# Optimization experiments

Hardware: AMD Instinct MI355X
Metric: run time of the kernel (lower is better)

The kernel has to match this reference:

```python
import jax, jax.numpy as jnp
import numpy as np

B, S, D, H = 4, 2048, 1024, 16
HD = D // H  # 64


def setup_inputs() -> dict:
    key = jax.random.key(0)
    k1, k2, k3, k4, k5 = jax.random.split(key, 5)
    scale = 0.02
    return {
        "hidden_states": jax.random.normal(k1, (B, S, D), dtype=jnp.float32),
        "c_attn_w": jax.random.normal(k2, (D, 3 * D), dtype=jnp.float32) * scale,
        "c_attn_b": jax.random.normal(k3, (3 * D,), dtype=jnp.float32) * scale,
        "c_proj_w": jax.random.normal(k4, (D, D), dtype=jnp.float32) * scale,
        "c_proj_b": jax.random.normal(k5, (D,), dtype=jnp.float32) * scale,
    }


def reference(hidden_states, c_attn_w, c_attn_b, c_proj_w, c_proj_b):
    b, s, d = hidden_states.shape
    # Conv1D: x @ W + b, fused QKV
    qkv = hidden_states @ c_attn_w + c_attn_b  # [b, s, 3d]
    q, k, v = jnp.split(qkv, 3, axis=-1)
    # split heads -> [b, h, s, hd]
    def split_heads(x):
        return x.reshape(b, s, H, HD).transpose(0, 2, 1, 3)
    q, k, v = split_heads(q), split_heads(k), split_heads(v)
    # scaled dot-product attention with causal mask (eager GPT-2 math)
    scores = jnp.einsum("bhqd,bhkd->bhqk", q, k) / jnp.asarray(HD ** 0.5, q.dtype)
    causal = jnp.tril(jnp.ones((s, s), dtype=bool))  # [s, s]
    mask_value = jnp.asarray(jnp.finfo(scores.dtype).min, scores.dtype)
    scores = jnp.where(causal[None, None, :, :], scores, mask_value)
    attn = jax.nn.softmax(scores, axis=-1)
    out = jnp.einsum("bhqk,bhkd->bhqd", attn, v)  # [b, h, s, hd]
    out = out.transpose(0, 2, 1, 3).reshape(b, s, d)  # merge heads
    out = out @ c_proj_w + c_proj_b
    return out
```

## Files before the change

kernel.cpp:

```cpp
#include <hip/hip_runtime.h>
#include <hip/hip_bf16.h>
#include <stdint.h>

#define B_ 4
#define S_ 2048
#define D_ 1024
#define H_ 16
#define HD_ 64

typedef __bf16 bf16_t;
typedef bf16_t bf16x8 __attribute__((ext_vector_type(8)));
typedef bf16_t bf16x4 __attribute__((ext_vector_type(4)));
typedef float f32x4 __attribute__((ext_vector_type(4)));
typedef float f32x16 __attribute__((ext_vector_type(16)));

__device__ __forceinline__ bf16x8 cvt8(f32x4 lo, f32x4 hi) {
  bf16x8 r;
#pragma unroll
  for (int i = 0; i < 4; i++) {
    r[i] = (bf16_t)lo[i];
    r[i + 4] = (bf16_t)hi[i];
  }
  return r;
}

__device__ __forceinline__ void async_lds16(const bf16_t* g, bf16_t* l) {
  __builtin_amdgcn_global_load_lds(
      (const __attribute__((address_space(1))) void*)g,
      (__attribute__((address_space(3))) void*)l, 16, 0, 0);
}

__device__ __forceinline__ uint32_t pk2(float a, float b) {
  union {
    bf16_t h[2];
    uint32_t u;
  } x;
  x.h[0] = (bf16_t)a;
  x.h[1] = (bf16_t)b;
  return x.u;
}

__device__ __forceinline__ void swap32(uint32_t& a, uint32_t& b) {
  asm("v_permlane32_swap_b32 %0, %1" : "+v"(a), "+v"(b));
}

union PAU {
  uint32_t w[4];
  bf16x8 v;
};

__global__ __launch_bounds__(256) void cvt_f32_bf16(
    const float* __restrict__ in, bf16_t* __restrict__ out) {
  size_t i = ((size_t)blockIdx.x * 256 + threadIdx.x) * 8;
  f32x4 lo = *(const f32x4*)(in + i);
  f32x4 hi = *(const f32x4*)(in + i + 4);
  *(bf16x8*)(out + i) = cvt8(lo, hi);
}

__global__ void transpose_cvt(const float* __restrict__ in,
                              bf16_t* __restrict__ out, int R, int C) {
  __shared__ bf16_t tile[32][33];
  int c0 = blockIdx.x * 32, r0 = blockIdx.y * 32;
  int tx = threadIdx.x, ty = threadIdx.y;
  for (int i = ty; i < 32; i += 8)
    tile[i][tx] = (bf16_t)in[(size_t)(r0 + i) * C + c0 + tx];
  __syncthreads();
  for (int i = ty; i < 32; i += 8)
    out[(size_t)(c0 + i) * R + r0 + tx] = tile[tx][i];
}

__global__ __launch_bounds__(256) void gemm_bt(
    const void* __restrict__ A, const bf16_t* __restrict__ BT,
    const float* __restrict__ bias, float* __restrict__ Cout,
    bf16_t* __restrict__ qws, bf16_t* __restrict__ kws,
    bf16_t* __restrict__ vws, int M, int Nw, int K, int mode, int a_is_f32,
    size_t a_off) {
  __shared__ bf16_t As[128 * 32];
  __shared__ bf16_t Bs[128 * 32];
  const int tid = threadIdx.x;
  const int wave = tid >> 6, lane = tid & 63;
  const int quad = lane >> 4, tn = lane & 15;
  const int m_blk = blockIdx.y * 128, n_blk = blockIdx.x * 128;
  const int wm = (wave >> 1) * 64, wn = (wave & 1) * 64;

  f32x4 acc[4][4] = {};

  const int srow = wave * 32 + (lane >> 2);
  const int scol = (lane & 3) * 8;
  size_t aoff = a_off + (size_t)(m_blk + srow) * K + scol;
  const bf16_t* gb = BT + (size_t)(n_blk + srow) * K + scol;
  bf16_t* lbB0 = &Bs[wave * 1024];
  bf16_t* lbB1 = &Bs[wave * 1024 + 512];
  bf16_t* laA0 = &As[wave * 1024];
  bf16_t* laA1 = &As[wave * 1024 + 512];

  for (int k0 = 0; k0 < K; k0 += 32) {
    async_lds16(gb, lbB0);
    async_lds16(gb + (size_t)16 * K, lbB1);
    if (a_is_f32) {
      const float* gaf = (const float*)A + aoff;
      f32x4 a00 = *(const f32x4*)gaf;
      f32x4 a01 = *(const f32x4*)(gaf + 4);
      f32x4 a10 = *(const f32x4*)(gaf + (size_t)16 * K);
      f32x4 a11 = *(const f32x4*)(gaf + (size_t)16 * K + 4);
      *(bf16x8*)&As[srow * 32 + scol] = cvt8(a00, a01);
      *(bf16x8*)&As[(srow + 16) * 32 + scol] = cvt8(a10, a11);
    } else {
      const bf16_t* ga = (const bf16_t*)A + aoff;
      async_lds16(ga, laA0);
      async_lds16(ga + (size_t)16 * K, laA1);
    }
    aoff += 32;
    gb += 32;
    __syncthreads();

    bf16x8 af[4], bfr[4];
#pragma unroll
    for (int i = 0; i < 4; i++)
      af[i] = *(const bf16x8*)&As[(wm + i * 16 + tn) * 32 + quad * 8];
#pragma unroll
    for (int i = 0; i < 4; i++)
      bfr[i] = *(const bf16x8*)&Bs[(wn + i * 16 + tn) * 32 + quad * 8];
#pragma unroll
    for (int mi = 0; mi < 4; mi++)
#pragma unroll
      for (int ni = 0; ni < 4; ni++)
        acc[mi][ni] = __builtin_amdgcn_mfma_f32_16x16x32_bf16(af[mi], bfr[ni],
                                                              acc[mi][ni], 0, 0, 0);
    __syncthreads();
  }

  if (mode == 0) {
#pragma unroll
    for (int ni = 0; ni < 4; ni++) {
      int n = n_blk + wn + ni * 16 + tn;
      float bv = bias[n];
#pragma unroll
      for (int mi = 0; mi < 4; mi++)
#pragma unroll
        for (int r = 0; r < 4; r++) {
          int m = m_blk + wm + mi * 16 + quad * 4 + r;
          Cout[(size_t)m * Nw + n] = acc[mi][ni][r] + bv;
        }
    }
  } else {
#pragma unroll
    for (int ni = 0; ni < 4; ni++) {
      int n = n_blk + wn + ni * 16 + tn;
      int sec = n >> 10;
      int hn = n & 1023;
      int hh = hn >> 6, hd = hn & 63;
      float bv = bias[n];
      if (sec == 2) {
#pragma unroll
        for (int mi = 0; mi < 4; mi++) {
          int m = m_blk + wm + mi * 16 + quad * 4;
          int bb = m >> 11, s = m & 2047;
          bf16x4 pk;
#pragma unroll
          for (int r = 0; r < 4; r++) pk[r] = (bf16_t)(acc[mi][ni][r] + bv);
          *(bf16x4*)&vws[((size_t)(bb * H_ + hh) * HD_ + hd) * S_ + s] = pk;
        }
      } else {
        bf16_t* dst = (sec == 0) ? qws : kws;
#pragma unroll
        for (int mi = 0; mi < 4; mi++)
#pragma unroll
          for (int r = 0; r < 4; r++) {
            int m = m_blk + wm + mi * 16 + quad * 4 + r;
            int bb = m >> 11, s = m & 2047;
            dst[((size_t)(bb * H_ + hh) * S_ + s) * HD_ + hd] =
                (bf16_t)(acc[mi][ni][r] + bv);
          }
      }
    }
  }
}

__global__ __launch_bounds__(512, 2) void attn_kernel(
    const bf16_t* __restrict__ Qw, const bf16_t* __restrict__ Kw,
    const bf16_t* __restrict__ VTw, bf16_t* __restrict__ Ow) {
  __shared__ bf16_t Ks[2][64 * 64];
  __shared__ bf16_t Vt[2][64 * 64];

  const int tid = threadIdx.x;
  const int wave = tid >> 6, lane = tid & 63;
  const int lq = lane & 31;
  const int h = lane >> 5;
  const int qoff = h * 4;
  const int bid = blockIdx.x;
  const int j = bid >> 3;
  const int bh = (bid & 7) * 8 + (j >> 2);
  const int pj = j & 3;

  const bf16_t* Qb = Qw + (size_t)bh * S_ * HD_;
  const bf16_t* Kb = Kw + (size_t)bh * S_ * HD_;
  const bf16_t* VTb = VTw + (size_t)bh * HD_ * S_;

  const float kScale = 0.125f * 1.44269504088896f;

  bf16x8 onesf;
#pragma unroll
  for (int jj = 0; jj < 8; jj++) onesf[jj] = (bf16_t)1.0f;

  const float NEG = -30000.0f;
  const int b = bh >> 4, hh = bh & 15;

  const int srow = wave * 8 + (lane >> 3);
  const int sslot = lane & 7;
  const bf16_t* kp = Kb + (size_t)srow * HD_ + (sslot ^ (srow & 7)) * 8;
  const bf16_t* vp = VTb + (size_t)srow * S_ + (sslot ^ (srow & 7)) * 8;

#define STAGE(buf, kt)                                                 \
  do {                                                                 \
    async_lds16(kp + (size_t)(kt) * (64 * HD_), &Ks[buf][wave * 512]); \
    async_lds16(vp + (size_t)(kt) * 64, &Vt[buf][wave * 512]);         \
  } while (0)

  for (int task = 0; task < 2; task++) {
    const int qt = task == 0 ? (7 - pj) : pj;
    const int qb = qt * 256;
    const int qa = qb + ((lq >> 3) << 6) + wave * 8 + (lq & 7);

    bf16x8 qf[4];
#pragma unroll
    for (int kg = 0; kg < 4; kg++) {
      bf16x8 v = *(const bf16x8*)&Qb[(size_t)qa * HD_ + kg * 16 + h * 8];
#pragma unroll
      for (int jj = 0; jj < 8; jj++) v[jj] = (bf16_t)((float)v[jj] * kScale);
      qf[kg] = v;
    }

    f32x16 o0 = {}, o1 = {};
    f32x16 ls = {};
    float mrow = NEG;

    const int kt_max = (qb + 255) >> 6;

    if (task) __syncthreads();
    STAGE(0, 0);

    for (int kt = 0; kt <= kt_max; kt++) {
      __syncthreads();
      if (kt < kt_max) STAGE((kt + 1) & 1, kt + 1);

      const bf16_t* KsB = Ks[kt & 1];
      const bf16_t* VtB = Vt[kt & 1];
      const int rsl = lq & 7;

      f32x16 st0 = {}, st1 = {};
      __builtin_amdgcn_s_setprio(1);
#pragma unroll
      for (int kg = 0; kg < 4; kg++) {
        const int slot = kg * 2 + h;
        bf16x8 kf0 = *(const bf16x8*)&KsB[lq * 64 + ((slot ^ rsl) * 8)];
        bf16x8 kf1 = *(const bf16x8*)&KsB[(32 + lq) * 64 + ((slot ^ rsl) * 8)];
        st0 = __builtin_amdgcn_mfma_f32_32x32x16_bf16(kf0, qf[kg], st0, 0, 0, 0);
        st1 = __builtin_amdgcn_mfma_f32_32x32x16_bf16(kf1, qf[kg], st1, 0, 0, 0);
      }
      __builtin_amdgcn_s_setprio(0);
      if (kt * 64 + 63 > qb) {
#pragma unroll
        for (int r = 0; r < 16; r++) {
          int key0 = kt * 64 + (r & 3) + 8 * (r >> 2) + qoff;
          if (key0 > qa) st0[r] = NEG;
          if (key0 + 32 > qa) st1[r] = NEG;
        }
      }
      float m8[8];
#pragma unroll
      for (int i = 0; i < 4; i++) {
        m8[i] = fmaxf(fmaxf(st0[4 * i], st0[4 * i + 1]),
                      fmaxf(st0[4 * i + 2], st0[4 * i + 3]));
        m8[4 + i] = fmaxf(fmaxf(st1[4 * i], st1[4 * i + 1]),
                          fmaxf(st1[4 * i + 2], st1[4 * i + 3]));
      }
      float mx = fmaxf(fmaxf(fmaxf(m8[0], m8[1]), fmaxf(m8[2], m8[3])),
                       fmaxf(fmaxf(m8[4], m8[5]), fmaxf(m8[6], m8[7])));
      mx = fmaxf(mx, __shfl_xor(mx, 32, 64));

      if (__any(mx > mrow + 8.f)) {
        float mnew = fmaxf(mrow, mx);
        float alpha = exp2f(mrow - mnew);
        mrow = mnew;
#pragma unroll
        for (int r = 0; r < 16; r++) {
          float ar = __shfl(alpha, (r & 3) + 8 * (r >> 2) + qoff, 64);
          o0[r] *= ar;
          o1[r] *= ar;
          ls[r] *= ar;
        }
      }
#pragma unroll
      for (int r = 0; r < 16; r++) {
        st0[r] = exp2f(st0[r] - mrow);
        st1[r] = exp2f(st1[r] - mrow);
      }

      PAU pa[4];
      {
        uint32_t w[8];
#pragma unroll
        for (int i = 0; i < 8; i++) w[i] = pk2(st0[2 * i], st0[2 * i + 1]);
        swap32(w[0], w[2]);
        swap32(w[1], w[3]);
        swap32(w[4], w[6]);
        swap32(w[5], w[7]);
        pa[0].w[0] = w[0]; pa[0].w[1] = w[1]; pa[0].w[2] = w[2]; pa[0].w[3] = w[3];
        pa[1].w[0] = w[4]; pa[1].w[1] = w[5]; pa[1].w[2] = w[6]; pa[1].w[3] = w[7];
#pragma unroll
        for (int i = 0; i < 8; i++) w[i] = pk2(st1[2 * i], st1[2 * i + 1]);
        swap32(w[0], w[2]);
        swap32(w[1], w[3]);
        swap32(w[4], w[6]);
        swap32(w[5], w[7]);
        pa[2].w[0] = w[0]; pa[2].w[1] = w[1]; pa[2].w[2] = w[2]; pa[2].w[3] = w[3];
        pa[3].w[0] = w[4]; pa[3].w[1] = w[5]; pa[3].w[2] = w[6]; pa[3].w[3] = w[7];
      }

      __builtin_amdgcn_s_setprio(1);
#pragma unroll
      for (int kg = 0; kg < 4; kg++) {
        const int slot = kg * 2 + h;
        bf16x8 vf0 = *(const bf16x8*)&VtB[lq * 64 + ((slot ^ rsl) * 8)];
        bf16x8 vf1 = *(const bf16x8*)&VtB[(32 + lq) * 64 + ((slot ^ rsl) * 8)];
        o0 = __builtin_amdgcn_mfma_f32_32x32x16_bf16(pa[kg].v, vf0, o0, 0, 0, 0);
        o1 = __builtin_amdgcn_mfma_f32_32x32x16_bf16(pa[kg].v, vf1, o1, 0, 0, 0);
        ls = __builtin_amdgcn_mfma_f32_32x32x16_bf16(pa[kg].v, onesf, ls, 0, 0, 0);
      }
      __builtin_amdgcn_s_setprio(0);
    }

#pragma unroll
    for (int r = 0; r < 16; r++) {
      int qr = (r & 3) + 8 * (r >> 2) + qoff;
      int q = qb + ((qr >> 3) << 6) + wave * 8 + (qr & 7);
      float inv = 1.f / fmaxf(ls[r], 1e-30f);
      bf16_t* dst = Ow + (size_t)(b * S_ + q) * D_ + hh * HD_;
      dst[lq] = (bf16_t)(o0[r] * inv);
      dst[32 + lq] = (bf16_t)(o1[r] * inv);
    }
  }
#undef STAGE
}

extern "C" void kernel_launch(void* const* d_in, const int* in_sizes, int n_in,
                              void* d_out, int out_size, void* d_ws,
                              size_t ws_size, hipStream_t stream) {
  const float* hidden = nullptr;
  const float* attn_w = nullptr;
  const float* attn_b = nullptr;
  const float* proj_w = nullptr;
  const float* proj_b = nullptr;
  for (int i = 0; i < n_in; ++i) {
    switch (in_sizes[i]) {
      case 8388608: hidden = (const float*)d_in[i]; break;
      case 3145728: attn_w = (const float*)d_in[i]; break;
      case 3072:    attn_b = (const float*)d_in[i]; break;
      case 1048576: proj_w = (const float*)d_in[i]; break;
      case 1024:    proj_b = (const float*)d_in[i]; break;
      default: break;
    }
  }
  if (!hidden) hidden = (const float*)d_in[0];
  if (!attn_w) attn_w = (const float*)d_in[1];
  if (!attn_b) attn_b = (const float*)d_in[2];
  if (!proj_w) proj_w = (const float*)d_in[3];
  if (!proj_b) proj_b = (const float*)d_in[4];
  float* out = (float*)d_out;

  char* ws = (char*)d_ws;
  const size_t AWS_B = (size_t)B_ * S_ * D_ * 2;
  const size_t QKV_E = (size_t)B_ * H_ * S_ * HD_;

  bf16_t* aws = (bf16_t*)ws;
  bf16_t* wT1 = (bf16_t*)ws;
  bf16_t* qws = (bf16_t*)(ws + AWS_B);
  bf16_t* kws = qws + QKV_E;
  bf16_t* vws = kws + QKV_E;
  bf16_t* wT2 = qws;
  bf16_t* hb = (bf16_t*)d_out;

  cvt_f32_bf16<<<dim3(4096), 256, 0, stream>>>(hidden, hb);
  transpose_cvt<<<dim3(96, 32), dim3(32, 8), 0, stream>>>(attn_w, wT1, 1024, 3072);
  gemm_bt<<<dim3(24, 64), 256, 0, stream>>>(
      hb, wT1, attn_b, nullptr, qws, kws, vws, 8192, 3072, 1024, 1, 0, 0);
  attn_kernel<<<dim3(256), 512, 0, stream>>>(qws, kws, vws, aws);
  transpose_cvt<<<dim3(32, 32), dim3(32, 8), 0, stream>>>(proj_w, wT2, 1024, 1024);
  gemm_bt<<<dim3(8, 64), 256, 0, stream>>>(
      aws, wT2, proj_b, out, nullptr, nullptr, nullptr, 8192, 1024, 1024, 0, 0, 0);
}
```

Baseline: 286.8 us.

## Rewrite GEMM as 256x128 tile with triple-buffered async LDS pipeline and swizzle

Replaces the 128x128, K=32 single-buffered GEMM with a 512-thread 256x128 tile kernel using K=64 steps and a three-stage async global-to-LDS pipeline. It adds an XOR swizzle on LDS columns to avoid bank conflicts, and uses fine-grained vmcnt waits plus raised wave priority around the MFMA blocks. The aim is to hide global load latency, halve barriers per unit of work and raise operand reuse. In exchange it uses much more LDS (about 144KB), which limits occupancy, and the proj GEMM launches only 256 blocks.

```diff
diff --git a/kernel.cpp b/kernel.cpp
--- a/kernel.cpp
+++ b/kernel.cpp
@@ -69,92 +69,125 @@
     out[(size_t)(c0 + i) * R + r0 + tx] = tile[tx][i];
 }
 
-__global__ __launch_bounds__(256) void gemm_bt(
-    const void* __restrict__ A, const bf16_t* __restrict__ BT,
+__global__ __launch_bounds__(512, 2) void gemm256(
+    const bf16_t* __restrict__ Ab, const bf16_t* __restrict__ Bb,
     const float* __restrict__ bias, float* __restrict__ Cout,
     bf16_t* __restrict__ qws, bf16_t* __restrict__ kws,
-    bf16_t* __restrict__ vws, int M, int Nw, int K, int mode, int a_is_f32,
-    size_t a_off) {
-  __shared__ bf16_t As[128 * 32];
-  __shared__ bf16_t Bs[128 * 32];
+    bf16_t* __restrict__ vws, int M, int Nw, int K, int mode) {
+  __shared__ bf16_t As[3 * 256 * 64];
+  __shared__ bf16_t Bs[3 * 128 * 64];
   const int tid = threadIdx.x;
   const int wave = tid >> 6, lane = tid & 63;
   const int quad = lane >> 4, tn = lane & 15;
-  const int m_blk = blockIdx.y * 128, n_blk = blockIdx.x * 128;
-  const int wm = (wave >> 1) * 64, wn = (wave & 1) * 64;
-
-  f32x4 acc[4][4] = {};
-
-  const int srow = wave * 32 + (lane >> 2);
-  const int scol = (lane & 3) * 8;
-  size_t aoff = a_off + (size_t)(m_blk + srow) * K + scol;
-  const bf16_t* gb = BT + (size_t)(n_blk + srow) * K + scol;
-  bf16_t* lbB0 = &Bs[wave * 1024];
-  bf16_t* lbB1 = &Bs[wave * 1024 + 512];
-  bf16_t* laA0 = &As[wave * 1024];
-  bf16_t* laA1 = &As[wave * 1024 + 512];
-
-  for (int k0 = 0; k0 < K; k0 += 32) {
-    async_lds16(gb, lbB0);
-    async_lds16(gb + (size_t)16 * K, lbB1);
-    if (a_is_f32) {
-      const float* gaf = (const float*)A + aoff;
-      f32x4 a00 = *(const f32x4*)gaf;
-      f32x4 a01 = *(const f32x4*)(gaf + 4);
-      f32x4 a10 = *(const f32x4*)(gaf + (size_t)16 * K);
-      f32x4 a11 = *(const f32x4*)(gaf + (size_t)16 * K + 4);
-      *(bf16x8*)&As[srow * 32 + scol] = cvt8(a00, a01);
-      *(bf16x8*)&As[(srow + 16) * 32 + scol] = cvt8(a10, a11);
-    } else {
-      const bf16_t* ga = (const bf16_t*)A + aoff;
-      async_lds16(ga, laA0);
-      async_lds16(ga + (size_t)16 * K, laA1);
-    }
-    aoff += 32;
-    gb += 32;
-    __syncthreads();
-
-    bf16x8 af[4], bfr[4];
-#pragma unroll
-    for (int i = 0; i < 4; i++)
-      af[i] = *(const bf16x8*)&As[(wm + i * 16 + tn) * 32 + quad * 8];
-#pragma unroll
-    for (int i = 0; i < 4; i++)
-      bfr[i] = *(const bf16x8*)&Bs[(wn + i * 16 + tn) * 32 + quad * 8];
-#pragma unroll
-    for (int mi = 0; mi < 4; mi++)
-#pragma unroll
-      for (int ni = 0; ni < 4; ni++)
-        acc[mi][ni] = __builtin_amdgcn_mfma_f32_16x16x32_bf16(af[mi], bfr[ni],
-                                                              acc[mi][ni], 0, 0, 0);
-    __syncthreads();
+  const int m_blk = blockIdx.y * 256, n_blk = blockIdx.x * 128;
+  const int wm = wave >> 2, wn = wave & 3;
+
+  f32x4 acc[8][2] = {};
+
+  const int sr = tid >> 3;
+  const int asw = ((tid & 7) ^ (sr & 7)) * 8;
+  const bf16_t* aS[4];
+  const bf16_t* bS[2];
+#pragma unroll
+  for (int c = 0; c < 4; c++)
+    aS[c] = Ab + (size_t)(m_blk + c * 64 + sr) * K + asw;
+#pragma unroll
+  for (int c = 0; c < 2; c++)
+    bS[c] = Bb + (size_t)(n_blk + c * 64 + sr) * K + asw;
+  bf16_t* aD[4];
+  bf16_t* bD[2];
+#pragma unroll
+  for (int c = 0; c < 4; c++) aD[c] = As + (size_t)(c * 512 + wave * 64) * 8;
+#pragma unroll
+  for (int c = 0; c < 2; c++) bD[c] = Bs + (size_t)(c * 512 + wave * 64) * 8;
+
+#define GSTAGE(st, jt)                                              \
+  do {                                                              \
+    _Pragma("unroll") for (int c = 0; c < 4; c++)                   \
+        async_lds16(aS[c] + (size_t)(jt) * 64, aD[c] + (st)*16384); \
+    _Pragma("unroll") for (int c = 0; c < 2; c++)                   \
+        async_lds16(bS[c] + (size_t)(jt) * 64, bD[c] + (st)*8192);  \
+  } while (0)
+
+  const int NT = K >> 6;
+
+  GSTAGE(0, 0);
+  GSTAGE(1, 1);
+  asm volatile("s_waitcnt vmcnt(6)" ::: "memory");
+  __builtin_amdgcn_s_barrier();
+  __builtin_amdgcn_sched_barrier(0);
+
+  int cur = 0;
+  for (int j = 0; j < NT; ++j) {
+    const int st2 = cur >= 1 ? cur - 1 : 2;
+    if (j + 2 < NT) GSTAGE(st2, j + 2);
+
+    const bf16_t* As_ = As + (size_t)cur * 16384;
+    const bf16_t* Bs_ = Bs + (size_t)cur * 8192;
+    __builtin_amdgcn_s_setprio(1);
+#pragma unroll
+    for (int ks = 0; ks < 2; ks++) {
+      bf16x8 af[8], bfv[2];
+#pragma unroll
+      for (int mi = 0; mi < 8; mi++) {
+        int row = wm * 128 + mi * 16 + tn;
+        af[mi] = *(const bf16x8*)&As_[row * 64 +
+                                      (((ks * 4 + quad) ^ (tn & 7)) * 8)];
+      }
+#pragma unroll
+      for (int ni = 0; ni < 2; ni++) {
+        int row = wn * 32 + ni * 16 + tn;
+        bfv[ni] = *(const bf16x8*)&Bs_[row * 64 +
+                                       (((ks * 4 + quad) ^ (tn & 7)) * 8)];
+      }
+#pragma unroll
+      for (int mi = 0; mi < 8; mi++)
+#pragma unroll
+        for (int ni = 0; ni < 2; ni++)
+          acc[mi][ni] = __builtin_amdgcn_mfma_f32_16x16x32_bf16(
+              af[mi], bfv[ni], acc[mi][ni], 0, 0, 0);
+    }
+    __builtin_amdgcn_s_setprio(0);
+
+    if (j + 1 < NT) {
+      asm volatile("s_waitcnt lgkmcnt(0)" ::: "memory");
+      __builtin_amdgcn_sched_barrier(0);
+      if (j + 2 < NT)
+        asm volatile("s_waitcnt vmcnt(6)" ::: "memory");
+      else
+        asm volatile("s_waitcnt vmcnt(0)" ::: "memory");
+      __builtin_amdgcn_s_barrier();
+      __builtin_amdgcn_sched_barrier(0);
+    }
+    cur = cur + 1 == 3 ? 0 : cur + 1;
   }
+#undef GSTAGE
 
   if (mode == 0) {
 #pragma unroll
-    for (int ni = 0; ni < 4; ni++) {
-      int n = n_blk + wn + ni * 16 + tn;
+    for (int ni = 0; ni < 2; ni++) {
+      int n = n_blk + wn * 32 + ni * 16 + tn;
       float bv = bias[n];
 #pragma unroll
-      for (int mi = 0; mi < 4; mi++)
+      for (int mi = 0; mi < 8; mi++)
 #pragma unroll
         for (int r = 0; r < 4; r++) {
-          int m = m_blk + wm + mi * 16 + quad * 4 + r;
+          int m = m_blk + wm * 128 + mi * 16 + quad * 4 + r;
           Cout[(size_t)m * Nw + n] = acc[mi][ni][r] + bv;
         }
     }
   } else {
 #pragma unroll
-    for (int ni = 0; ni < 4; ni++) {
-      int n = n_blk + wn + ni * 16 + tn;
+    for (int ni = 0; ni < 2; ni++) {
+      int n = n_blk + wn * 32 + ni * 16 + tn;
       int sec = n >> 10;
       int hn = n & 1023;
       int hh = hn >> 6, hd = hn & 63;
       float bv = bias[n];
       if (sec == 2) {
 #pragma unroll
-        for (int mi = 0; mi < 4; mi++) {
-          int m = m_blk + wm + mi * 16 + quad * 4;
+        for (int mi = 0; mi < 8; mi++) {
+          int m = m_blk + wm * 128 + mi * 16 + quad * 4;
           int bb = m >> 11, s = m & 2047;
           bf16x4 pk;
 #pragma unroll
@@ -164,10 +197,10 @@
       } else {
         bf16_t* dst = (sec == 0) ? qws : kws;
 #pragma unroll
-        for (int mi = 0; mi < 4; mi++)
+        for (int mi = 0; mi < 8; mi++)
 #pragma unroll
           for (int r = 0; r < 4; r++) {
-            int m = m_blk + wm + mi * 16 + quad * 4 + r;
+            int m = m_blk + wm * 128 + mi * 16 + quad * 4 + r;
             int bb = m >> 11, s = m & 2047;
             dst[((size_t)(bb * H_ + hh) * S_ + s) * HD_ + hd] =
                 (bf16_t)(acc[mi][ni][r] + bv);
@@ -383,10 +416,10 @@
 
   cvt_f32_bf16<<<dim3(4096), 256, 0, stream>>>(hidden, hb);
   transpose_cvt<<<dim3(96, 32), dim3(32, 8), 0, stream>>>(attn_w, wT1, 1024, 3072);
-  gemm_bt<<<dim3(24, 64), 256, 0, stream>>>(
-      hb, wT1, attn_b, nullptr, qws, kws, vws, 8192, 3072, 1024, 1, 0, 0);
+  gemm256<<<dim3(24, 32), 512, 0, stream>>>(
+      hb, wT1, attn_b, nullptr, qws, kws, vws, 8192, 3072, 1024, 1);
   attn_kernel<<<dim3(256), 512, 0, stream>>>(qws, kws, vws, aws);
   transpose_cvt<<<dim3(32, 32), dim3(32, 8), 0, stream>>>(proj_w, wT2, 1024, 1024);
-  gemm_bt<<<dim3(8, 64), 256, 0, stream>>>(
-      aws, wT2, proj_b, out, nullptr, nullptr, nullptr, 8192, 1024, 1024, 0, 0, 0);
-}
+  gemm256<<<dim3(8, 32), 512, 0, stream>>>(
+      aws, wT2, proj_b, out, nullptr, nullptr, nullptr, 8192, 1024, 1024, 0);
+}
```

After: 303.6 us. 5.8% more time.
